# Kernel optimization log

Hardware: AMD Instinct MI355X
Metric: run time of the kernel (lower is better)

Reference implementation:

```python
import jax, jax.numpy as jnp
import numpy as np

B, D = 16384, 512
EPS_COS = 1e-8  # torch cosine_similarity eps


def setup_inputs() -> dict:
    key = jax.random.key(0)
    ks = jax.random.split(key, 8)
    rep1 = jax.random.normal(ks[0], (B, D), jnp.float32)
    rep2 = jax.random.normal(ks[1], (B, D), jnp.float32)
    rep3 = jax.random.normal(ks[2], (B, D), jnp.float32)
    hazard = jax.random.normal(ks[3], (B, 1), jnp.float32)
    # F.nll_loss expects log-probabilities
    score = jax.nn.log_softmax(jax.random.normal(ks[4], (B, 2), jnp.float32), axis=-1)
    time = jax.random.uniform(ks[5], (B,), jnp.float32)
    event = jax.random.randint(ks[6], (B,), 0, 2, dtype=jnp.int32)
    perm = jax.random.permutation(ks[7], B)  # deterministic stand-in for shuffle()
    x1_idx = perm[: B // 2].astype(jnp.int32)
    x2_idx = perm[B // 2 :].astype(jnp.int32)
    return dict(rep1=rep1, rep2=rep2, rep3=rep3, hazard=hazard, score=score,
                time=time, event=event, x1_idx=x1_idx, x2_idx=x2_idx)


def _normalize(r):
    n = jnp.maximum(jnp.linalg.norm(r, axis=-1, keepdims=True), EPS_COS)
    return r / n


def reference(rep1, rep2, rep3, hazard, score, time, event, x1_idx, x2_idx):
    trade_off, margin, alpha, beta = 0.3, 0.2, 0.5, 0.5
    ev_f = event.astype(score.dtype)

    # ---- cross-entropy term: F.nll_loss(log_probs, event) ----
    nll = -jnp.mean(jnp.take_along_axis(score, event[:, None].astype(jnp.int32), axis=1))

    # ---- Cox negative log-likelihood ----
    order = jnp.argsort(-time)            # descending time
    risk = hazard[order, 0]               # [B]
    evs = ev_f[order]
    log_risk = jnp.log(jnp.cumsum(jnp.exp(risk)) + 1e-6)
    cox = -jnp.sum((risk - log_risk) * evs) / (jnp.sum(evs) + 1e-6)

    # ---- contrastive loss (3 modalities, vectorized over pairs) ----
    R = jnp.stack([_normalize(rep1), _normalize(rep2), _normalize(rep3)])  # [M,B,D]
    x = R[:, x1_idx]  # [M,P,D]
    y = R[:, x2_idx]  # [M,P,D]
    pairs = [(0, 1), (0, 2), (1, 2)]
    dis_xx = sum((x[i] * x[j]).sum(-1) for i, j in pairs)  # [P]
    dis_yy = sum((y[i] * y[j]).sum(-1) for i, j in pairs)  # [P]
    dis_xy = (x * y).sum(-1).sum(0)                         # [P]
    con = jnp.mean(jnp.log1p(jnp.exp(margin + dis_xy - alpha * dis_xx - beta * dis_yy)))

    return nll + cox + trade_off * con
```

## Files before the change

### kernel.cpp

```cpp
#include <hip/hip_runtime.h>
#include <math.h>

#define B_N     16384
#define D_N     512
#define NPAIR   8192
#define NBUCKET 8192
#define CON_BLOCKS 2048
#define STAT_BLOCKS 64
#define BIG_BLOCKS (CON_BLOCKS + STAT_BLOCKS)
#define COX_BLOCKS 64
#define POISON_U   0xAAAAAAAAu

__device__ __forceinline__ float wave_reduce(float v) {
    #pragma unroll
    for (int m = 32; m >= 1; m >>= 1) v += __shfl_xor(v, m, 64);
    return v;
}

__device__ __forceinline__ float dot4(float4 a, float4 b) {
    return a.x*b.x + a.y*b.y + a.z*b.z + a.w*b.w;
}

__device__ __forceinline__ int bucket_of(float t) {
    return min(max((int)(t * 8192.0f), 0), NBUCKET - 1);
}

__device__ __forceinline__ unsigned long long key_of(float t, int i) {
    return (((unsigned long long)__float_as_uint(t)) << 14) |
           (unsigned long long)(B_N - 1 - i);
}

__global__ __launch_bounds__(256) void k_big(
        const float* __restrict__ rep1,
        const float* __restrict__ rep2,
        const float* __restrict__ rep3,
        const float* __restrict__ hazard,
        const float* __restrict__ score,
        const float* __restrict__ time,
        const int*   __restrict__ event,
        const int*   __restrict__ x1_idx,
        const int*   __restrict__ x2_idx,
        float* __restrict__ partCon,
        float* __restrict__ partNll,
        float* __restrict__ partEv,
        float* __restrict__ sumE,
        int*   __restrict__ head,
        int*   __restrict__ next)
{
    __shared__ float sh0[4], sh1[4];
    const int tid  = threadIdx.x;
    const int lane = tid & 63;
    const int wave = tid >> 6;

    if (blockIdx.x < CON_BLOCKS) {
        const int p  = blockIdx.x * 4 + wave;
        const int ia = x1_idx[p];
        const int ib = x2_idx[p];
        const float4* A1 = (const float4*)(rep1 + (size_t)ia * D_N);
        const float4* A2 = (const float4*)(rep2 + (size_t)ia * D_N);
        const float4* A3 = (const float4*)(rep3 + (size_t)ia * D_N);
        const float4* B1 = (const float4*)(rep1 + (size_t)ib * D_N);
        const float4* B2 = (const float4*)(rep2 + (size_t)ib * D_N);
        const float4* B3 = (const float4*)(rep3 + (size_t)ib * D_N);

        float v[15];
        #pragma unroll
        for (int k = 0; k < 15; ++k) v[k] = 0.f;
        #pragma unroll
        for (int r = 0; r < 2; ++r) {
            const int k = lane + r * 64;
            float4 a1 = A1[k], a2 = A2[k], a3 = A3[k];
            float4 b1 = B1[k], b2 = B2[k], b3 = B3[k];
            v[0]  += dot4(a1, a1); v[1]  += dot4(a2, a2); v[2]  += dot4(a3, a3);
            v[3]  += dot4(b1, b1); v[4]  += dot4(b2, b2); v[5]  += dot4(b3, b3);
            v[6]  += dot4(a1, a2); v[7]  += dot4(a1, a3); v[8]  += dot4(a2, a3);
            v[9]  += dot4(b1, b2); v[10] += dot4(b1, b3); v[11] += dot4(b2, b3);
            v[12] += dot4(a1, b1); v[13] += dot4(a2, b2); v[14] += dot4(a3, b3);
        }
        #pragma unroll
        for (int k = 0; k < 15; ++k) v[k] = wave_reduce(v[k]);

        if (lane == 0) {
            float n1a = fmaxf(sqrtf(v[0]), 1e-8f), n2a = fmaxf(sqrtf(v[1]), 1e-8f), n3a = fmaxf(sqrtf(v[2]), 1e-8f);
            float n1b = fmaxf(sqrtf(v[3]), 1e-8f), n2b = fmaxf(sqrtf(v[4]), 1e-8f), n3b = fmaxf(sqrtf(v[5]), 1e-8f);
            float dxx = v[6]/(n1a*n2a) + v[7]/(n1a*n3a) + v[8]/(n2a*n3a);
            float dyy = v[9]/(n1b*n2b) + v[10]/(n1b*n3b) + v[11]/(n2b*n3b);
            float dxy = v[12]/(n1a*n1b) + v[13]/(n2a*n2b) + v[14]/(n3a*n3b);
            float s = 0.2f + dxy - 0.5f*dxx - 0.5f*dyy;
            sh0[wave] = log1pf(expf(s));
        }
        __syncthreads();
        if (tid == 0)
            partCon[blockIdx.x] = sh0[0] + sh0[1] + sh0[2] + sh0[3];
    } else {
        const int sb = blockIdx.x - CON_BLOCKS;
        const int i  = sb * 256 + tid;
        const float t = time[i];
        const float e = __expf(hazard[i]);
        const int   b = bucket_of(t);
        atomicAdd(&sumE[b], e);
        const int old = atomicExch(&head[b], i + 1);
        next[i] = old;

        const int ev = event[i];
        float nll_p = wave_reduce(score[i * 2 + ev]);
        float ev_p  = wave_reduce((float)ev);
        if (lane == 0) { sh0[wave] = nll_p; sh1[wave] = ev_p; }
        __syncthreads();
        if (tid == 0) {
            partNll[sb] = sh0[0] + sh0[1] + sh0[2] + sh0[3];
            partEv[sb]  = sh1[0] + sh1[1] + sh1[2] + sh1[3];
        }
    }
}

__global__ __launch_bounds__(256) void k_cox(
        const float* __restrict__ hazard,
        const float* __restrict__ time,
        const int*   __restrict__ event,
        const int*   __restrict__ head,
        const int*   __restrict__ next,
        const float* __restrict__ sumE,
        const float* __restrict__ partCon,
        const float* __restrict__ partNll,
        const float* __restrict__ partEv,
        float* __restrict__ partCox,
        unsigned* __restrict__ doneCox,
        float* __restrict__ out)
{
    __shared__ float cumL[NBUCKET];
    __shared__ float psum[256];
    __shared__ float shX[4];
    __shared__ int lastflag;
    const int tid  = threadIdx.x;
    const int lane = tid & 63;
    const int wave = tid >> 6;

    const int base = tid * 32;
    float fs = 0.f;
    #pragma unroll
    for (int k = 0; k < 32; ++k) fs += sumE[base + k];
    psum[tid] = fs;
    __syncthreads();
    for (int d = 1; d < 256; d <<= 1) {
        float v = (tid >= d) ? psum[tid - d] : 0.f;
        __syncthreads();
        psum[tid] += v;
        __syncthreads();
    }
    const float total = psum[255];
    float run = total - psum[tid];
    #pragma unroll
    for (int k = 31; k >= 0; --k) {
        cumL[k * 256 + tid] = run;
        run += sumE[base + k];
    }
    __syncthreads();

    const int i = blockIdx.x * 256 + tid;
    const float t = time[i];
    const float h = hazard[i];
    const int   b = bucket_of(t);
    const unsigned long long ki = key_of(t, i);

    float cum = cumL[(b & 31) * 256 + (b >> 5)] + __expf(h);
    int p = head[b];
    while (p >= 1 && p <= B_N) {
        const int j = p - 1;
        const float tj = time[j];
        if (key_of(tj, j) > ki) cum += __expf(hazard[j]);
        p = next[j];
    }
    float cox_p = event[i] ? (h - logf(cum + 1e-6f)) : 0.f;
    cox_p = wave_reduce(cox_p);
    if (lane == 0) shX[wave] = cox_p;
    __syncthreads();
    if (tid == 0)
        atomicExch(&partCox[blockIdx.x], shX[0] + shX[1] + shX[2] + shX[3]);

    __threadfence();
    if (tid == 0)
        lastflag = (atomicAdd(doneCox, 1u) == POISON_U + (COX_BLOCKS - 1));
    __syncthreads();
    if (lastflag) {
        float con = 0.f;
        #pragma unroll
        for (int k = 0; k < CON_BLOCKS / 256; ++k) con += partCon[tid + k * 256];
        float cox = 0.f, nll = 0.f, ev = 0.f;
        if (tid < COX_BLOCKS) {
            cox = atomicAdd(&partCox[tid], 0.f);
            nll = partNll[tid];
            ev  = partEv[tid];
        }
        con = wave_reduce(con);
        cox = wave_reduce(cox);
        nll = wave_reduce(nll);
        ev  = wave_reduce(ev);
        __syncthreads();
        if (lane == 0) { shX[wave] = con; }
        __syncthreads();
        float C = shX[0] + shX[1] + shX[2] + shX[3];
        if (lane == 0) { shX[wave] = cox; }
        __syncthreads();
        float X = shX[0] + shX[1] + shX[2] + shX[3];
        if (lane == 0) { shX[wave] = nll; }
        __syncthreads();
        float N = shX[0] + shX[1] + shX[2] + shX[3];
        if (lane == 0) { shX[wave] = ev; }
        __syncthreads();
        float E = shX[0] + shX[1] + shX[2] + shX[3];
        if (tid == 0)
            out[0] = (-N / (float)B_N) + (-X / (E + 1e-6f)) + 0.3f * (C / (float)NPAIR);
    }
}

extern "C" void kernel_launch(void* const* d_in, const int* in_sizes, int n_in,
                              void* d_out, int out_size, void* d_ws, size_t ws_size,
                              hipStream_t stream)
{
    const float* rep1   = (const float*)d_in[0];
    const float* rep2   = (const float*)d_in[1];
    const float* rep3   = (const float*)d_in[2];
    const float* hazard = (const float*)d_in[3];
    const float* score  = (const float*)d_in[4];
    const float* time_  = (const float*)d_in[5];
    const int*   event  = (const int*)d_in[6];
    const int*   x1     = (const int*)d_in[7];
    const int*   x2     = (const int*)d_in[8];
    float* out = (float*)d_out;

    char* w = (char*)d_ws;
    float*    sumE    = (float*)   (w + 0);
    int*      head    = (int*)     (w + 32768);
    unsigned* doneCox = (unsigned*)(w + 65536);
    int*      next    = (int*)     (w + 65600);
    float*    partCon = (float*)   (w + 131136);
    float*    partNll = (float*)   (w + 139328);
    float*    partEv  = (float*)   (w + 139584);
    float*    partCox = (float*)   (w + 139840);

    k_big <<<BIG_BLOCKS, 256, 0, stream>>>(rep1, rep2, rep3, hazard, score, time_,
                                           event, x1, x2, partCon, partNll, partEv,
                                           sumE, head, next);
    k_cox <<<COX_BLOCKS, 256, 0, stream>>>(hazard, time_, event, head, next, sumE,
                                           partCon, partNll, partEv, partCox,
                                           doneCox, out);
}
```

Measured before the change: 145.6 us.

## Split stats/scan into small kernels and fuse Cox walk with contrastive blocks

Moves the bucket-building and NLL stats into a small first kernel and the bucket prefix scan into a single-block kernel writing a global cumulative array. The Cox chain-walk blocks are then launched in the same grid as the contrastive pair blocks, so the latency-bound Cox phase overlaps with the bandwidth-bound contrastive reads, and each Cox block no longer redoes the full 8192-bucket scan in shared memory. This adds one extra kernel launch and serial small kernels before the big one, and the last-block completion counter now covers all fused blocks.

```diff
diff --git a/kernel.cpp b/kernel.cpp
--- a/kernel.cpp
+++ b/kernel.cpp
@@ -5,10 +5,10 @@
 #define D_N     512
 #define NPAIR   8192
 #define NBUCKET 8192
+#define COX_BLOCKS 64
 #define CON_BLOCKS 2048
+#define FUSE_BLOCKS (COX_BLOCKS + CON_BLOCKS)
 #define STAT_BLOCKS 64
-#define BIG_BLOCKS (CON_BLOCKS + STAT_BLOCKS)
-#define COX_BLOCKS 64
 #define POISON_U   0xAAAAAAAAu
 
 __device__ __forceinline__ float wave_reduce(float v) {
@@ -30,17 +30,11 @@
            (unsigned long long)(B_N - 1 - i);
 }
 
-__global__ __launch_bounds__(256) void k_big(
-        const float* __restrict__ rep1,
-        const float* __restrict__ rep2,
-        const float* __restrict__ rep3,
+__global__ __launch_bounds__(256) void k_stats(
         const float* __restrict__ hazard,
         const float* __restrict__ score,
         const float* __restrict__ time,
         const int*   __restrict__ event,
-        const int*   __restrict__ x1_idx,
-        const int*   __restrict__ x2_idx,
-        float* __restrict__ partCon,
         float* __restrict__ partNll,
         float* __restrict__ partEv,
         float* __restrict__ sumE,
@@ -51,9 +45,81 @@
     const int tid  = threadIdx.x;
     const int lane = tid & 63;
     const int wave = tid >> 6;
-
-    if (blockIdx.x < CON_BLOCKS) {
-        const int p  = blockIdx.x * 4 + wave;
+    const int sb   = blockIdx.x;
+    const int i    = sb * 256 + tid;
+
+    const float t = time[i];
+    const float e = __expf(hazard[i]);
+    const int   b = bucket_of(t);
+    atomicAdd(&sumE[b], e);
+    const int old = atomicExch(&head[b], i + 1);
+    next[i] = old;
+
+    const int ev = event[i];
+    float nll_p = wave_reduce(score[i * 2 + ev]);
+    float ev_p  = wave_reduce((float)ev);
+    if (lane == 0) { sh0[wave] = nll_p; sh1[wave] = ev_p; }
+    __syncthreads();
+    if (tid == 0) {
+        partNll[sb] = sh0[0] + sh0[1] + sh0[2] + sh0[3];
+        partEv[sb]  = sh1[0] + sh1[1] + sh1[2] + sh1[3];
+    }
+}
+
+__global__ __launch_bounds__(256) void k_scan(
+        const float* __restrict__ sumE,
+        float* __restrict__ cumG)
+{
+    __shared__ float psum[256];
+    const int tid  = threadIdx.x;
+    const int base = tid * 32;
+    float fs = 0.f;
+    #pragma unroll
+    for (int k = 0; k < 32; ++k) fs += sumE[base + k];
+    psum[tid] = fs;
+    __syncthreads();
+    for (int d = 1; d < 256; d <<= 1) {
+        float v = (tid >= d) ? psum[tid - d] : 0.f;
+        __syncthreads();
+        psum[tid] += v;
+        __syncthreads();
+    }
+    const float total = psum[255];
+    float run = total - psum[tid];
+    #pragma unroll
+    for (int k = 31; k >= 0; --k) {
+        cumG[base + k] = run;
+        run += sumE[base + k];
+    }
+}
+
+__global__ __launch_bounds__(256) void k_fused(
+        const float* __restrict__ rep1,
+        const float* __restrict__ rep2,
+        const float* __restrict__ rep3,
+        const float* __restrict__ hazard,
+        const float* __restrict__ time,
+        const int*   __restrict__ event,
+        const int*   __restrict__ x1_idx,
+        const int*   __restrict__ x2_idx,
+        const int*   __restrict__ head,
+        const int*   __restrict__ next,
+        const float* __restrict__ cumG,
+        const float* __restrict__ partNll,
+        const float* __restrict__ partEv,
+        float* __restrict__ partCon,
+        float* __restrict__ partCox,
+        unsigned* __restrict__ doneAll,
+        float* __restrict__ out)
+{
+    __shared__ float shX[4];
+    __shared__ int lastflag;
+    const int tid  = threadIdx.x;
+    const int lane = tid & 63;
+    const int wave = tid >> 6;
+
+    if (blockIdx.x >= COX_BLOCKS) {
+        const int p  = (blockIdx.x - COX_BLOCKS) * 4 + wave;
         const int ia = x1_idx[p];
         const int ib = x2_idx[p];
         const float4* A1 = (const float4*)(rep1 + (size_t)ia * D_N);
@@ -87,105 +153,43 @@
             float dyy = v[9]/(n1b*n2b) + v[10]/(n1b*n3b) + v[11]/(n2b*n3b);
             float dxy = v[12]/(n1a*n1b) + v[13]/(n2a*n2b) + v[14]/(n3a*n3b);
             float s = 0.2f + dxy - 0.5f*dxx - 0.5f*dyy;
-            sh0[wave] = log1pf(expf(s));
+            shX[wave] = log1pf(expf(s));
         }
         __syncthreads();
         if (tid == 0)
-            partCon[blockIdx.x] = sh0[0] + sh0[1] + sh0[2] + sh0[3];
+            atomicExch(&partCon[blockIdx.x - COX_BLOCKS], shX[0] + shX[1] + shX[2] + shX[3]);
     } else {
-        const int sb = blockIdx.x - CON_BLOCKS;
-        const int i  = sb * 256 + tid;
+        const int i = blockIdx.x * 256 + tid;
         const float t = time[i];
-        const float e = __expf(hazard[i]);
+        const float h = hazard[i];
         const int   b = bucket_of(t);
-        atomicAdd(&sumE[b], e);
-        const int old = atomicExch(&head[b], i + 1);
-        next[i] = old;
-
-        const int ev = event[i];
-        float nll_p = wave_reduce(score[i * 2 + ev]);
-        float ev_p  = wave_reduce((float)ev);
-        if (lane == 0) { sh0[wave] = nll_p; sh1[wave] = ev_p; }
-        __syncthreads();
-        if (tid == 0) {
-            partNll[sb] = sh0[0] + sh0[1] + sh0[2] + sh0[3];
-            partEv[sb]  = sh1[0] + sh1[1] + sh1[2] + sh1[3];
-        }
-    }
-}
-
-__global__ __launch_bounds__(256) void k_cox(
-        const float* __restrict__ hazard,
-        const float* __restrict__ time,
-        const int*   __restrict__ event,
-        const int*   __restrict__ head,
-        const int*   __restrict__ next,
-        const float* __restrict__ sumE,
-        const float* __restrict__ partCon,
-        const float* __restrict__ partNll,
-        const float* __restrict__ partEv,
-        float* __restrict__ partCox,
-        unsigned* __restrict__ doneCox,
-        float* __restrict__ out)
-{
-    __shared__ float cumL[NBUCKET];
-    __shared__ float psum[256];
-    __shared__ float shX[4];
-    __shared__ int lastflag;
-    const int tid  = threadIdx.x;
-    const int lane = tid & 63;
-    const int wave = tid >> 6;
-
-    const int base = tid * 32;
-    float fs = 0.f;
-    #pragma unroll
-    for (int k = 0; k < 32; ++k) fs += sumE[base + k];
-    psum[tid] = fs;
-    __syncthreads();
-    for (int d = 1; d < 256; d <<= 1) {
-        float v = (tid >= d) ? psum[tid - d] : 0.f;
-        __syncthreads();
-        psum[tid] += v;
-        __syncthreads();
-    }
-    const float total = psum[255];
-    float run = total - psum[tid];
-    #pragma unroll
-    for (int k = 31; k >= 0; --k) {
-        cumL[k * 256 + tid] = run;
-        run += sumE[base + k];
-    }
-    __syncthreads();
-
-    const int i = blockIdx.x * 256 + tid;
-    const float t = time[i];
-    const float h = hazard[i];
-    const int   b = bucket_of(t);
-    const unsigned long long ki = key_of(t, i);
-
-    float cum = cumL[(b & 31) * 256 + (b >> 5)] + __expf(h);
-    int p = head[b];
-    while (p >= 1 && p <= B_N) {
-        const int j = p - 1;
-        const float tj = time[j];
-        if (key_of(tj, j) > ki) cum += __expf(hazard[j]);
-        p = next[j];
-    }
-    float cox_p = event[i] ? (h - logf(cum + 1e-6f)) : 0.f;
-    cox_p = wave_reduce(cox_p);
-    if (lane == 0) shX[wave] = cox_p;
-    __syncthreads();
-    if (tid == 0)
-        atomicExch(&partCox[blockIdx.x], shX[0] + shX[1] + shX[2] + shX[3]);
+        const unsigned long long ki = key_of(t, i);
+
+        float cum = cumG[b] + __expf(h);
+        int p = head[b];
+        while (p >= 1 && p <= B_N) {
+            const int j = p - 1;
+            const float tj = time[j];
+            if (key_of(tj, j) > ki) cum += __expf(hazard[j]);
+            p = next[j];
+        }
+        float cox_p = event[i] ? (h - logf(cum + 1e-6f)) : 0.f;
+        cox_p = wave_reduce(cox_p);
+        if (lane == 0) shX[wave] = cox_p;
+        __syncthreads();
+        if (tid == 0)
+            atomicExch(&partCox[blockIdx.x], shX[0] + shX[1] + shX[2] + shX[3]);
+    }
 
     __threadfence();
     if (tid == 0)
-        lastflag = (atomicAdd(doneCox, 1u) == POISON_U + (COX_BLOCKS - 1));
+        lastflag = (atomicAdd(doneAll, 1u) == POISON_U + (FUSE_BLOCKS - 1));
     __syncthreads();
     if (lastflag) {
         float con = 0.f;
         #pragma unroll
-        for (int k = 0; k < CON_BLOCKS / 256; ++k) con += partCon[tid + k * 256];
+        for (int k = 0; k < CON_BLOCKS / 256; ++k)
+            con += atomicAdd(&partCon[tid + k * 256], 0.f);
         float cox = 0.f, nll = 0.f, ev = 0.f;
         if (tid < COX_BLOCKS) {
             cox = atomicAdd(&partCox[tid], 0.f);
@@ -232,17 +236,19 @@
     char* w = (char*)d_ws;
     float*    sumE    = (float*)   (w + 0);
     int*      head    = (int*)     (w + 32768);
-    unsigned* doneCox = (unsigned*)(w + 65536);
+    unsigned* doneAll = (unsigned*)(w + 65536);
     int*      next    = (int*)     (w + 65600);
     float*    partCon = (float*)   (w + 131136);
     float*    partNll = (float*)   (w + 139328);
     float*    partEv  = (float*)   (w + 139584);
     float*    partCox = (float*)   (w + 139840);
-
-    k_big <<<BIG_BLOCKS, 256, 0, stream>>>(rep1, rep2, rep3, hazard, score, time_,
-                                           event, x1, x2, partCon, partNll, partEv,
-                                           sumE, head, next);
-    k_cox <<<COX_BLOCKS, 256, 0, stream>>>(hazard, time_, event, head, next, sumE,
-                                           partCon, partNll, partEv, partCox,
-                                           doneCox, out);
-}
+    float*    cumG    = (float*)   (w + 140096);
+
+    k_stats <<<STAT_BLOCKS, 256, 0, stream>>>(hazard, score, time_, event,
+                                              partNll, partEv, sumE, head, next);
+    k_scan  <<<1, 256, 0, stream>>>(sumE, cumG);
+    k_fused <<<FUSE_BLOCKS, 256, 0, stream>>>(rep1, rep2, rep3, hazard, time_, event,
+                                              x1, x2, head, next, cumG,
+                                              partNll, partEv, partCon, partCox,
+                                              doneAll, out);
+}
```

Result: slower. 422.2 us (+190.0%).
